# Kernel tuning notes

Measured on AMD Instinct MI355X. Metric: run time of the kernel, lower is better.

Reference implementation:

```python
import jax, jax.numpy as jnp
import numpy as np

N_NODES = 50000
N_GRAPHS = 256

def _gcn_layer(h, src, dst, W, b, n_nodes):
    # GCNConv: linear transform, add self-loops, symmetric deg^-1/2 norm, scatter-add, bias
    h = h @ W  # [N, C_out]
    loop = jnp.arange(n_nodes, dtype=src.dtype)
    src_f = jnp.concatenate([src, loop])
    dst_f = jnp.concatenate([dst, loop])
    ones = jnp.ones_like(dst_f, dtype=h.dtype)
    deg = jax.ops.segment_sum(ones, dst_f, num_segments=n_nodes)  # includes self-loops
    dinv = jnp.where(deg > 0, jax.lax.rsqrt(deg), 0.0)
    norm = dinv[src_f] * dinv[dst_f]  # [E+N]
    msg = h[src_f] * norm[:, None]
    out = jax.ops.segment_sum(msg, dst_f, num_segments=n_nodes)
    return out + b


def setup_inputs() -> dict:
    key = jax.random.key(0)
    ks = jax.random.split(key, 12)
    d_in, d_hid, nhid, nout = 128, 128, 256, 768
    x = jax.random.normal(ks[0], (N_NODES, d_in), dtype=jnp.float32)
    edge_index = jax.random.randint(ks[1], (2, 800000), 0, N_NODES, dtype=jnp.int64)
    batch = jnp.sort(jax.random.randint(ks[2], (N_NODES,), 0, N_GRAPHS, dtype=jnp.int64))
    def lin(k, fan_in, fan_out):
        lim = 1.0 / np.sqrt(fan_in)
        kw, kb = jax.random.split(k)
        W = jax.random.uniform(kw, (fan_in, fan_out), jnp.float32, -lim, lim)
        b = jax.random.uniform(kb, (fan_out,), jnp.float32, -lim, lim)
        return W, b
    W1, b1 = lin(ks[3], d_in, d_hid)
    W2, b2 = lin(ks[4], d_hid, d_hid)
    W3, b3 = lin(ks[5], d_hid, d_hid)
    Wm1, bm1 = lin(ks[6], d_hid, nhid)
    Wm2, bm2 = lin(ks[7], nhid, nout)
    return {"x": x, "edge_index": edge_index, "batch": batch,
            "W1": W1, "b1": b1, "W2": W2, "b2": b2, "W3": W3, "b3": b3,
            "Wm1": Wm1, "bm1": bm1, "Wm2": Wm2, "bm2": bm2}


def reference(x, edge_index, batch, W1, b1, W2, b2, W3, b3, Wm1, bm1, Wm2, bm2):
    src, dst = edge_index[0], edge_index[1]
    n = x.shape[0]
    h = jax.nn.relu(_gcn_layer(x, src, dst, W1, b1, n))
    h = jax.nn.relu(_gcn_layer(h, src, dst, W2, b2, n))
    h = _gcn_layer(h, src, dst, W3, b3, n)  # no relu before pooling (matches source)
    # global mean pool over graphs
    sums = jax.ops.segment_sum(h, batch, num_segments=N_GRAPHS)
    cnts = jax.ops.segment_sum(jnp.ones((n,), h.dtype), batch, num_segments=N_GRAPHS)
    pooled = sums / jnp.clip(cnts, 1.0)[:, None]  # [G, d_hid]
    out = jax.nn.relu(pooled @ Wm1 + bm1)
    out = out @ Wm2 + bm2  # [G, nout]
    return out
```

## Files before the change

kernel.cpp:

```cpp
#include <hip/hip_runtime.h>
#include <hip/hip_bf16.h>

using bf16 = __hip_bfloat16;
typedef __attribute__((ext_vector_type(8))) short bf16x8;
typedef __attribute__((ext_vector_type(4))) float f32x4;

__device__ __forceinline__ float lo2f(unsigned u) { return __uint_as_float(u << 16); }
__device__ __forceinline__ float hi2f(unsigned u) { return __uint_as_float(u & 0xffff0000u); }
__device__ __forceinline__ unsigned pack_bf2(float a, float b) {
    bf16 t0 = __float2bfloat16(a), t1 = __float2bfloat16(b);
    return (unsigned)*(unsigned short*)&t0 | ((unsigned)*(unsigned short*)&t1 << 16);
}

#define CAP 64
#define NPART 8
#define NCHUNK 256

__global__ __launch_bounds__(256)
void fill_pad(const int* __restrict__ ei, int E, int N,
              int* __restrict__ cursor, int* __restrict__ colPad)
{
    int part  = blockIdx.x & (NPART - 1);
    int chunk = blockIdx.x >> 3;
    int lo = (int)(((long long)N * part) >> 3);
    int hi = (int)(((long long)N * (part + 1)) >> 3);
    int csz = (E + NCHUNK - 1) / NCHUNK;
    int beg = chunk * csz;
    int end = min(beg + csz, E);
    const int* __restrict__ dstp = ei + E;
    for (int e = beg + (int)threadIdx.x; e < end; e += 256) {
        int d = __builtin_nontemporal_load(dstp + e);
        if (d >= lo && d < hi) {
            int s = __builtin_nontemporal_load(ei + e);
            int p = atomicAdd(&cursor[d], 1);
            if (p < CAP) colPad[(d << 6) + p] = s;
        }
    }
}

__global__ __launch_bounds__(256)
void dinv_gstart(const int* __restrict__ cursor, int N, float* __restrict__ dinv,
                 const int* __restrict__ batch, int* __restrict__ gstart, int G)
{
    int i = blockIdx.x * 256 + threadIdx.x;
    if (i >= N) return;
    dinv[i] = rsqrtf((float)(cursor[i] + 1));
    int b = batch[i];
    int bp = (i == 0) ? -1 : batch[i - 1];
    for (int q = bp + 1; q <= b; ++q) gstart[q] = i;
    if (i == N - 1)
        for (int q = b + 1; q <= G; ++q) gstart[q] = N;
}

#define LDK 136

__global__ __launch_bounds__(256)
void gemm1_f32(const float* __restrict__ x, const float* __restrict__ W,
               const float* __restrict__ dinv, int N, bf16* __restrict__ g)
{
    __shared__ short Wt[128 * LDK];
    for (int i = threadIdx.x; i < 128 * 128; i += 256) {
        int k = i >> 7, n = i & 127;
        bf16 b = __float2bfloat16(W[i]);
        Wt[n * LDK + k] = *(short*)&b;
    }
    __syncthreads();

    int wave = threadIdx.x >> 6;
    int lane = threadIdx.x & 63;
    int ln   = lane & 15;
    int quad = lane >> 4;
    int m0 = (blockIdx.x * 4 + wave) * 16;
    if (m0 >= N) return;

    int row = m0 + ln;
    if (row >= N) row = N - 1;
    const float* hrow = x + (size_t)row * 128;

    bf16x8 a[4];
#pragma unroll
    for (int kk = 0; kk < 4; ++kk) {
        float4 f0 = *(const float4*)(hrow + kk * 32 + quad * 8);
        float4 f1 = *(const float4*)(hrow + kk * 32 + quad * 8 + 4);
        float fv[8] = {f0.x, f0.y, f0.z, f0.w, f1.x, f1.y, f1.z, f1.w};
#pragma unroll
        for (int j = 0; j < 8; ++j) {
            bf16 tb = __float2bfloat16(fv[j]);
            ((short*)&a[kk])[j] = *(short*)&tb;
        }
    }

    f32x4 c[8];
#pragma unroll
    for (int nt = 0; nt < 8; ++nt) c[nt] = (f32x4){0.f, 0.f, 0.f, 0.f};
#pragma unroll
    for (int kk = 0; kk < 4; ++kk)
#pragma unroll
        for (int nt = 0; nt < 8; ++nt) {
            bf16x8 b = *(const bf16x8*)&Wt[(nt * 16 + ln) * LDK + kk * 32 + quad * 8];
            c[nt] = __builtin_amdgcn_mfma_f32_16x16x32_bf16(a[kk], b, c[nt], 0, 0, 0);
        }
#pragma unroll
    for (int r = 0; r < 4; ++r) {
        int m = m0 + quad * 4 + r;
        if (m < N) {
            float dv = dinv[m];
#pragma unroll
            for (int nt = 0; nt < 8; ++nt) {
                bf16 val = __float2bfloat16(c[nt][r] * dv);
                ((unsigned short*)g)[(size_t)m * 128 + nt * 16 + ln] = *(unsigned short*)&val;
            }
        }
    }
}

__global__ __launch_bounds__(256)
void gemm_mfma(const bf16* __restrict__ hin, const float* __restrict__ W,
               const float* __restrict__ dinv, int N, bf16* __restrict__ g)
{
    __shared__ short Wt[128 * LDK];
    for (int i = threadIdx.x; i < 128 * 128; i += 256) {
        int k = i >> 7, n = i & 127;
        bf16 b = __float2bfloat16(W[i]);
        Wt[n * LDK + k] = *(short*)&b;
    }
    __syncthreads();

    int wave = threadIdx.x >> 6;
    int lane = threadIdx.x & 63;
    int ln   = lane & 15;
    int quad = lane >> 4;
    int m0 = (blockIdx.x * 4 + wave) * 16;
    if (m0 >= N) return;

    int row = m0 + ln;
    if (row >= N) row = N - 1;
    const short* hrow = (const short*)hin + (size_t)row * 128;

    bf16x8 a[4];
#pragma unroll
    for (int kk = 0; kk < 4; ++kk)
        a[kk] = *(const bf16x8*)(hrow + kk * 32 + quad * 8);

    f32x4 c[8];
#pragma unroll
    for (int nt = 0; nt < 8; ++nt) c[nt] = (f32x4){0.f, 0.f, 0.f, 0.f};
#pragma unroll
    for (int kk = 0; kk < 4; ++kk)
#pragma unroll
        for (int nt = 0; nt < 8; ++nt) {
            bf16x8 b = *(const bf16x8*)&Wt[(nt * 16 + ln) * LDK + kk * 32 + quad * 8];
            c[nt] = __builtin_amdgcn_mfma_f32_16x16x32_bf16(a[kk], b, c[nt], 0, 0, 0);
        }
#pragma unroll
    for (int r = 0; r < 4; ++r) {
        int m = m0 + quad * 4 + r;
        if (m < N) {
            float dv = dinv[m];
#pragma unroll
            for (int nt = 0; nt < 8; ++nt) {
                bf16 val = __float2bfloat16(c[nt][r] * dv);
                ((unsigned short*)g)[(size_t)m * 128 + nt * 16 + ln] = *(unsigned short*)&val;
            }
        }
    }
}

__global__ __launch_bounds__(256)
void gather16(const bf16* __restrict__ g, const int* __restrict__ cnt,
              const int* __restrict__ colPad, const float* __restrict__ dinv,
              const float* __restrict__ bias, int N, int do_relu, bf16* __restrict__ hout)
{
    int v = blockIdx.x * 4 + (threadIdx.x >> 6);
    if (v >= N) return;
    int lane = threadIdx.x & 63;
    const unsigned* gp = (const unsigned*)g;

    unsigned su = gp[(size_t)v * 64 + lane];
    float s0 = lo2f(su), s1 = hi2f(su);

    int beg = v << 6;
    int end = beg + min(cnt[v], CAP);
    const int* __restrict__ col = colPad;
    int i = beg;
    for (; i + 8 <= end; i += 8) {
        int cc[8];
#pragma unroll
        for (int j = 0; j < 8; ++j) cc[j] = col[i + j];
        unsigned uu[8];
#pragma unroll
        for (int j = 0; j < 8; ++j) uu[j] = gp[(size_t)cc[j] * 64 + lane];
#pragma unroll
        for (int j = 0; j < 8; ++j) { s0 += lo2f(uu[j]); s1 += hi2f(uu[j]); }
    }
    for (; i + 4 <= end; i += 4) {
        int c0 = col[i], c1 = col[i + 1], c2 = col[i + 2], c3 = col[i + 3];
        unsigned u0 = gp[(size_t)c0 * 64 + lane];
        unsigned u1 = gp[(size_t)c1 * 64 + lane];
        unsigned u2 = gp[(size_t)c2 * 64 + lane];
        unsigned u3 = gp[(size_t)c3 * 64 + lane];
        s0 += lo2f(u0) + lo2f(u1) + lo2f(u2) + lo2f(u3);
        s1 += hi2f(u0) + hi2f(u1) + hi2f(u2) + hi2f(u3);
    }
    for (; i < end; ++i) {
        unsigned u = gp[(size_t)col[i] * 64 + lane];
        s0 += lo2f(u);
        s1 += hi2f(u);
    }
    float dv = dinv[v];
    float2 bb = ((const float2*)bias)[lane];
    float r0 = fmaf(dv, s0, bb.x);
    float r1 = fmaf(dv, s1, bb.y);
    if (do_relu) { r0 = fmaxf(r0, 0.f); r1 = fmaxf(r1, 0.f); }
    ((unsigned*)hout)[(size_t)v * 64 + lane] = pack_bf2(r0, r1);
}

#define PCH 32
__global__ __launch_bounds__(128)
void pool_part(const bf16* __restrict__ h, const int* __restrict__ batch, int N,
               float* __restrict__ pooled)
{
    int c0 = blockIdx.x * PCH;
    if (c0 >= N) return;
    int f = threadIdx.x;
    int end = min(c0 + PCH, N);
    int cur = batch[c0];
    float acc = 0.f;
    for (int v = c0; v < end; ++v) {
        int b = batch[v];
        if (b != cur) {
            atomicAdd(&pooled[cur * 128 + f], acc);
            acc = 0.f;
            cur = b;
        }
        acc += __bfloat162float(h[(size_t)v * 128 + f]);
    }
    atomicAdd(&pooled[cur * 128 + f], acc);
}

__global__ __launch_bounds__(256)
void mlp1g(const float* __restrict__ pooled, const int* __restrict__ gstart,
           const float* __restrict__ Wm1, const float* __restrict__ bm1,
           float* __restrict__ O)
{
    __shared__ float Ps[128];
    int gg = blockIdx.x, j = threadIdx.x;
    if (j < 128) {
        int c = gstart[gg + 1] - gstart[gg];
        Ps[j] = pooled[gg * 128 + j] / (float)(c > 0 ? c : 1);
    }
    __syncthreads();
    float s = 0.f;
#pragma unroll 4
    for (int k = 0; k < 128; ++k) s = fmaf(Ps[k], Wm1[k * 256 + j], s);
    O[(size_t)gg * 256 + j] = fmaxf(s + bm1[j], 0.f);
}

__global__ __launch_bounds__(768)
void mlp2g(const float* __restrict__ O, const float* __restrict__ Wm2,
           const float* __restrict__ bm2, float* __restrict__ out)
{
    __shared__ float Os[256];
    int gg = blockIdx.x, j = threadIdx.x;
    if (j < 256) Os[j] = O[(size_t)gg * 256 + j];
    __syncthreads();
    float s = 0.f;
#pragma unroll 4
    for (int k = 0; k < 256; ++k) s = fmaf(Os[k], Wm2[k * 768 + j], s);
    out[(size_t)gg * 768 + j] = s + bm2[j];
}

extern "C" void kernel_launch(void* const* d_in, const int* in_sizes, int n_in,
                              void* d_out, int out_size, void* d_ws, size_t ws_size,
                              hipStream_t stream)
{
    const float* x     = (const float*)d_in[0];
    const int*   ei    = (const int*)d_in[1];
    const int*   batch = (const int*)d_in[2];
    const float *W1 = (const float*)d_in[3],  *bb1 = (const float*)d_in[4];
    const float *W2 = (const float*)d_in[5],  *bb2 = (const float*)d_in[6];
    const float *W3 = (const float*)d_in[7],  *bb3 = (const float*)d_in[8];
    const float *Wm1 = (const float*)d_in[9],  *bm1 = (const float*)d_in[10];
    const float *Wm2 = (const float*)d_in[11], *bm2 = (const float*)d_in[12];

    const int N = in_sizes[2];
    const int E = in_sizes[1] / 2;
    const int G = out_size / 768;

    char* wp = (char*)d_ws;
    bf16* bufG   = (bf16*)wp;  wp += (size_t)N * 128 * 2;
    bf16* bufH   = (bf16*)wp;  wp += (size_t)N * 128 * 2;
    int*  colPad = (int*)wp;   wp += (size_t)N * CAP * 4;
    int*  cursor = (int*)wp;   wp += (size_t)N * 4;
    float* pooled= (float*)wp; wp += (size_t)G * 128 * 4;
    float* dinv  = (float*)wp; wp += (size_t)N * 4;
    int*  gstart = (int*)wp;   wp += (size_t)(G + 1) * 4;
    float* Obuf  = (float*)wp; wp += (size_t)G * 256 * 4;

    hipMemsetAsync(cursor, 0, (size_t)N * 4 + (size_t)G * 128 * 4, stream);

    const int SB = (N + 255) / 256;
    const int gemm_grid   = (N + 63) / 64;
    const int gather_grid = (N + 3) / 4;

    fill_pad<<<NPART * NCHUNK, 256, 0, stream>>>(ei, E, N, cursor, colPad);
    dinv_gstart<<<SB, 256, 0, stream>>>(cursor, N, dinv, batch, gstart, G);

    gemm1_f32<<<gemm_grid, 256, 0, stream>>>(x, W1, dinv, N, bufG);
    gather16<<<gather_grid, 256, 0, stream>>>(bufG, cursor, colPad, dinv, bb1, N, 1, bufH);
    gemm_mfma<<<gemm_grid, 256, 0, stream>>>(bufH, W2, dinv, N, bufG);
    gather16<<<gather_grid, 256, 0, stream>>>(bufG, cursor, colPad, dinv, bb2, N, 1, bufH);
    gemm_mfma<<<gemm_grid, 256, 0, stream>>>(bufH, W3, dinv, N, bufG);
    gather16<<<gather_grid, 256, 0, stream>>>(bufG, cursor, colPad, dinv, bb3, N, 0, bufH);

    pool_part<<<(N + PCH - 1) / PCH, 128, 0, stream>>>(bufH, batch, N, pooled);
    mlp1g<<<G, 256, 0, stream>>>(pooled, gstart, Wm1, bm1, Obuf);
    mlp2g<<<G, 768, 0, stream>>>(Obuf, Wm2, bm2, (float*)d_out);
}
```

Before: 321.4 us.

## Fuse neighbor aggregation with GEMM by aggregating before the linear transform

Reorders each GCN layer to aggregate dinv-scaled features first and then multiply by W, using A(XW) = (AX)W. This lets the gather and the MFMA GEMM run in one kernel, with each wave aggregating 16 rows into LDS before its matmul. A small scale0 kernel pre-scales x by dinv and casts it to bf16. The aim is to drop three launches and the per-layer bf16 intermediate round trip through global memory. The cost is fewer, longer-running blocks, since each wave gathers 16 nodes serially and the larger LDS use limits occupancy, which may hurt latency hiding for the irregular gathers.

```diff
diff --git a/kernel.cpp b/kernel.cpp
--- a/kernel.cpp
+++ b/kernel.cpp
@@ -52,13 +52,33 @@
         for (int q = b + 1; q <= G; ++q) gstart[q] = N;
 }
 
+__global__ __launch_bounds__(256)
+void scale0(const float* __restrict__ x, const float* __restrict__ dinv,
+            int N, bf16* __restrict__ u)
+{
+    int v = blockIdx.x * 8 + (threadIdx.x >> 5);
+    if (v >= N) return;
+    int l = threadIdx.x & 31;
+    float dv = dinv[v];
+    float4 xx = *(const float4*)(x + (size_t)v * 128 + l * 4);
+    uint2 o;
+    o.x = pack_bf2(xx.x * dv, xx.y * dv);
+    o.y = pack_bf2(xx.z * dv, xx.w * dv);
+    ((uint2*)((unsigned*)u + (size_t)v * 64))[l] = o;
+}
+
 #define LDK 136
-
-__global__ __launch_bounds__(256)
-void gemm1_f32(const float* __restrict__ x, const float* __restrict__ W,
-               const float* __restrict__ dinv, int N, bf16* __restrict__ g)
+#define LDA 68
+
+__global__ __launch_bounds__(256)
+void aggemm(const bf16* __restrict__ uin, const int* __restrict__ cnt,
+            const int* __restrict__ colPad, const float* __restrict__ dinv,
+            const float* __restrict__ W, const float* __restrict__ bias,
+            int N, int do_relu, int out_u, bf16* __restrict__ out)
 {
     __shared__ short Wt[128 * LDK];
+    __shared__ unsigned aggbuf[64 * LDA];
+
     for (int i = threadIdx.x; i < 128 * 128; i += 256) {
         int k = i >> 7, n = i & 127;
         bf16 b = __float2bfloat16(W[i]);
@@ -68,27 +88,56 @@
 
     int wave = threadIdx.x >> 6;
     int lane = threadIdx.x & 63;
+    int m0 = blockIdx.x * 64;
+    const unsigned* up = (const unsigned*)uin;
+
+    for (int i = 0; i < 16; ++i) {
+        int v = m0 + wave * 16 + i;
+        unsigned outw = 0u;
+        if (v < N) {
+            unsigned su = up[(size_t)v * 64 + lane];
+            float s0 = lo2f(su), s1 = hi2f(su);
+            int beg = v << 6;
+            int end = beg + min(cnt[v], CAP);
+            const int* __restrict__ col = colPad;
+            int e = beg;
+            for (; e + 8 <= end; e += 8) {
+                int cc[8];
+#pragma unroll
+                for (int j = 0; j < 8; ++j) cc[j] = col[e + j];
+                unsigned uu[8];
+#pragma unroll
+                for (int j = 0; j < 8; ++j) uu[j] = up[(size_t)cc[j] * 64 + lane];
+#pragma unroll
+                for (int j = 0; j < 8; ++j) { s0 += lo2f(uu[j]); s1 += hi2f(uu[j]); }
+            }
+            for (; e + 4 <= end; e += 4) {
+                int c0 = col[e], c1 = col[e + 1], c2 = col[e + 2], c3 = col[e + 3];
+                unsigned u0 = up[(size_t)c0 * 64 + lane];
+                unsigned u1 = up[(size_t)c1 * 64 + lane];
+                unsigned u2 = up[(size_t)c2 * 64 + lane];
+                unsigned u3 = up[(size_t)c3 * 64 + lane];
+                s0 += lo2f(u0) + lo2f(u1) + lo2f(u2) + lo2f(u3);
+                s1 += hi2f(u0) + hi2f(u1) + hi2f(u2) + hi2f(u3);
+            }
+            for (; e < end; ++e) {
+                unsigned u = up[(size_t)col[e] * 64 + lane];
+                s0 += lo2f(u);
+                s1 += hi2f(u);
+            }
+            outw = pack_bf2(s0, s1);
+        }
+        aggbuf[(wave * 16 + i) * LDA + lane] = outw;
+    }
+
     int ln   = lane & 15;
     int quad = lane >> 4;
-    int m0 = (blockIdx.x * 4 + wave) * 16;
-    if (m0 >= N) return;
-
-    int row = m0 + ln;
-    if (row >= N) row = N - 1;
-    const float* hrow = x + (size_t)row * 128;
 
     bf16x8 a[4];
 #pragma unroll
-    for (int kk = 0; kk < 4; ++kk) {
-        float4 f0 = *(const float4*)(hrow + kk * 32 + quad * 8);
-        float4 f1 = *(const float4*)(hrow + kk * 32 + quad * 8 + 4);
-        float fv[8] = {f0.x, f0.y, f0.z, f0.w, f1.x, f1.y, f1.z, f1.w};
-#pragma unroll
-        for (int j = 0; j < 8; ++j) {
-            bf16 tb = __float2bfloat16(fv[j]);
-            ((short*)&a[kk])[j] = *(short*)&tb;
-        }
-    }
+    for (int kk = 0; kk < 4; ++kk)
+        a[kk] = *(const bf16x8*)((const short*)aggbuf +
+                                 (wave * 16 + ln) * (LDA * 2) + kk * 32 + quad * 8);
 
     f32x4 c[8];
 #pragma unroll
@@ -100,119 +149,22 @@
             bf16x8 b = *(const bf16x8*)&Wt[(nt * 16 + ln) * LDK + kk * 32 + quad * 8];
             c[nt] = __builtin_amdgcn_mfma_f32_16x16x32_bf16(a[kk], b, c[nt], 0, 0, 0);
         }
+
 #pragma unroll
     for (int r = 0; r < 4; ++r) {
-        int m = m0 + quad * 4 + r;
+        int m = m0 + wave * 16 + quad * 4 + r;
         if (m < N) {
             float dv = dinv[m];
 #pragma unroll
             for (int nt = 0; nt < 8; ++nt) {
-                bf16 val = __float2bfloat16(c[nt][r] * dv);
-                ((unsigned short*)g)[(size_t)m * 128 + nt * 16 + ln] = *(unsigned short*)&val;
-            }
-        }
-    }
-}
-
-__global__ __launch_bounds__(256)
-void gemm_mfma(const bf16* __restrict__ hin, const float* __restrict__ W,
-               const float* __restrict__ dinv, int N, bf16* __restrict__ g)
-{
-    __shared__ short Wt[128 * LDK];
-    for (int i = threadIdx.x; i < 128 * 128; i += 256) {
-        int k = i >> 7, n = i & 127;
-        bf16 b = __float2bfloat16(W[i]);
-        Wt[n * LDK + k] = *(short*)&b;
-    }
-    __syncthreads();
-
-    int wave = threadIdx.x >> 6;
-    int lane = threadIdx.x & 63;
-    int ln   = lane & 15;
-    int quad = lane >> 4;
-    int m0 = (blockIdx.x * 4 + wave) * 16;
-    if (m0 >= N) return;
-
-    int row = m0 + ln;
-    if (row >= N) row = N - 1;
-    const short* hrow = (const short*)hin + (size_t)row * 128;
-
-    bf16x8 a[4];
-#pragma unroll
-    for (int kk = 0; kk < 4; ++kk)
-        a[kk] = *(const bf16x8*)(hrow + kk * 32 + quad * 8);
-
-    f32x4 c[8];
-#pragma unroll
-    for (int nt = 0; nt < 8; ++nt) c[nt] = (f32x4){0.f, 0.f, 0.f, 0.f};
-#pragma unroll
-    for (int kk = 0; kk < 4; ++kk)
-#pragma unroll
-        for (int nt = 0; nt < 8; ++nt) {
-            bf16x8 b = *(const bf16x8*)&Wt[(nt * 16 + ln) * LDK + kk * 32 + quad * 8];
-            c[nt] = __builtin_amdgcn_mfma_f32_16x16x32_bf16(a[kk], b, c[nt], 0, 0, 0);
-        }
-#pragma unroll
-    for (int r = 0; r < 4; ++r) {
-        int m = m0 + quad * 4 + r;
-        if (m < N) {
-            float dv = dinv[m];
-#pragma unroll
-            for (int nt = 0; nt < 8; ++nt) {
-                bf16 val = __float2bfloat16(c[nt][r] * dv);
-                ((unsigned short*)g)[(size_t)m * 128 + nt * 16 + ln] = *(unsigned short*)&val;
-            }
-        }
-    }
-}
-
-__global__ __launch_bounds__(256)
-void gather16(const bf16* __restrict__ g, const int* __restrict__ cnt,
-              const int* __restrict__ colPad, const float* __restrict__ dinv,
-              const float* __restrict__ bias, int N, int do_relu, bf16* __restrict__ hout)
-{
-    int v = blockIdx.x * 4 + (threadIdx.x >> 6);
-    if (v >= N) return;
-    int lane = threadIdx.x & 63;
-    const unsigned* gp = (const unsigned*)g;
-
-    unsigned su = gp[(size_t)v * 64 + lane];
-    float s0 = lo2f(su), s1 = hi2f(su);
-
-    int beg = v << 6;
-    int end = beg + min(cnt[v], CAP);
-    const int* __restrict__ col = colPad;
-    int i = beg;
-    for (; i + 8 <= end; i += 8) {
-        int cc[8];
-#pragma unroll
-        for (int j = 0; j < 8; ++j) cc[j] = col[i + j];
-        unsigned uu[8];
-#pragma unroll
-        for (int j = 0; j < 8; ++j) uu[j] = gp[(size_t)cc[j] * 64 + lane];
-#pragma unroll
-        for (int j = 0; j < 8; ++j) { s0 += lo2f(uu[j]); s1 += hi2f(uu[j]); }
-    }
-    for (; i + 4 <= end; i += 4) {
-        int c0 = col[i], c1 = col[i + 1], c2 = col[i + 2], c3 = col[i + 3];
-        unsigned u0 = gp[(size_t)c0 * 64 + lane];
-        unsigned u1 = gp[(size_t)c1 * 64 + lane];
-        unsigned u2 = gp[(size_t)c2 * 64 + lane];
-        unsigned u3 = gp[(size_t)c3 * 64 + lane];
-        s0 += lo2f(u0) + lo2f(u1) + lo2f(u2) + lo2f(u3);
-        s1 += hi2f(u0) + hi2f(u1) + hi2f(u2) + hi2f(u3);
-    }
-    for (; i < end; ++i) {
-        unsigned u = gp[(size_t)col[i] * 64 + lane];
-        s0 += lo2f(u);
-        s1 += hi2f(u);
-    }
-    float dv = dinv[v];
-    float2 bb = ((const float2*)bias)[lane];
-    float r0 = fmaf(dv, s0, bb.x);
-    float r1 = fmaf(dv, s1, bb.y);
-    if (do_relu) { r0 = fmaxf(r0, 0.f); r1 = fmaxf(r1, 0.f); }
-    ((unsigned*)hout)[(size_t)v * 64 + lane] = pack_bf2(r0, r1);
+                float t = fmaf(dv, c[nt][r], bias[nt * 16 + ln]);
+                if (do_relu) t = fmaxf(t, 0.f);
+                if (out_u)   t *= dv;
+                bf16 val = __float2bfloat16(t);
+                ((unsigned short*)out)[(size_t)m * 128 + nt * 16 + ln] = *(unsigned short*)&val;
+            }
+        }
+    }
 }
 
 #define PCH 32
@@ -288,8 +240,8 @@
     const int G = out_size / 768;
 
     char* wp = (char*)d_ws;
-    bf16* bufG   = (bf16*)wp;  wp += (size_t)N * 128 * 2;
-    bf16* bufH   = (bf16*)wp;  wp += (size_t)N * 128 * 2;
+    bf16* bufA   = (bf16*)wp;  wp += (size_t)N * 128 * 2;
+    bf16* bufB   = (bf16*)wp;  wp += (size_t)N * 128 * 2;
     int*  colPad = (int*)wp;   wp += (size_t)N * CAP * 4;
     int*  cursor = (int*)wp;   wp += (size_t)N * 4;
     float* pooled= (float*)wp; wp += (size_t)G * 128 * 4;
@@ -300,20 +252,18 @@
     hipMemsetAsync(cursor, 0, (size_t)N * 4 + (size_t)G * 128 * 4, stream);
 
     const int SB = (N + 255) / 256;
-    const int gemm_grid   = (N + 63) / 64;
-    const int gather_grid = (N + 3) / 4;
+    const int agg_grid = (N + 63) / 64;
 
     fill_pad<<<NPART * NCHUNK, 256, 0, stream>>>(ei, E, N, cursor, colPad);
     dinv_gstart<<<SB, 256, 0, stream>>>(cursor, N, dinv, batch, gstart, G);
 
-    gemm1_f32<<<gemm_grid, 256, 0, stream>>>(x, W1, dinv, N, bufG);
-    gather16<<<gather_grid, 256, 0, stream>>>(bufG, cursor, colPad, dinv, bb1, N, 1, bufH);
-    gemm_mfma<<<gemm_grid, 256, 0, stream>>>(bufH, W2, dinv, N, bufG);
-    gather16<<<gather_grid, 256, 0, stream>>>(bufG, cursor, colPad, dinv, bb2, N, 1, bufH);
-    gemm_mfma<<<gemm_grid, 256, 0, stream>>>(bufH, W3, dinv, N, bufG);
-    gather16<<<gather_grid, 256, 0, stream>>>(bufG, cursor, colPad, dinv, bb3, N, 0, bufH);
-
-    pool_part<<<(N + PCH - 1) / PCH, 128, 0, stream>>>(bufH, batch, N, pooled);
+    scale0<<<(N + 7) / 8, 256, 0, stream>>>(x, dinv, N, bufA);
+
+    aggemm<<<agg_grid, 256, 0, stream>>>(bufA, cursor, colPad, dinv, W1, bb1, N, 1, 1, bufB);
+    aggemm<<<agg_grid, 256, 0, stream>>>(bufB, cursor, colPad, dinv, W2, bb2, N, 1, 1, bufA);
+    aggemm<<<agg_grid, 256, 0, stream>>>(bufA, cursor, colPad, dinv, W3, bb3, N, 0, 0, bufB);
+
+    pool_part<<<(N + PCH - 1) / PCH, 128, 0, stream>>>(bufB, batch, N, pooled);
     mlp1g<<<G, 256, 0, stream>>>(pooled, gstart, Wm1, bm1, Obuf);
     mlp2g<<<G, 768, 0, stream>>>(Obuf, Wm2, bm2, (float*)d_out);
 }
```

Measured after the change: 476.5 us. +48.3%, slower.

## Split neighbor gather into four feature-quarter passes with nontemporal index loads

Applied to the files above, without the earlier changes.

The gather is split into four launches, each covering a 32-feature quarter of every node. In each launch a 16-lane group handles one node, so the gathered working set per pass is 64-byte slices, which may fit better in L2/MALL. Column index loads and output stores are made nontemporal so they do not evict feature data from cache. In exchange, each pass re-reads the whole padded index list, a 64-byte slice under-uses each 128-byte line, and there are three extra launches per layer.

```diff
diff --git a/kernel.cpp b/kernel.cpp
--- a/kernel.cpp
+++ b/kernel.cpp
@@ -167,16 +167,20 @@
 }
 
 __global__ __launch_bounds__(256)
-void gather16(const bf16* __restrict__ g, const int* __restrict__ cnt,
+void gather4q(const bf16* __restrict__ g, const int* __restrict__ cnt,
               const int* __restrict__ colPad, const float* __restrict__ dinv,
-              const float* __restrict__ bias, int N, int do_relu, bf16* __restrict__ hout)
-{
-    int v = blockIdx.x * 4 + (threadIdx.x >> 6);
+              const float* __restrict__ bias, int N, int do_relu, int pass,
+              bf16* __restrict__ hout)
+{
+    int tid = threadIdx.x;
+    int grp = tid >> 4;
+    int l   = tid & 15;
+    int v   = blockIdx.x * 16 + grp;
     if (v >= N) return;
-    int lane = threadIdx.x & 63;
     const unsigned* gp = (const unsigned*)g;
-
-    unsigned su = gp[(size_t)v * 64 + lane];
+    int qoff = pass * 16 + l;
+
+    unsigned su = gp[(size_t)v * 64 + qoff];
     float s0 = lo2f(su), s1 = hi2f(su);
 
     int beg = v << 6;
@@ -186,33 +190,37 @@
     for (; i + 8 <= end; i += 8) {
         int cc[8];
 #pragma unroll
-        for (int j = 0; j < 8; ++j) cc[j] = col[i + j];
+        for (int j = 0; j < 8; ++j) cc[j] = __builtin_nontemporal_load(col + i + j);
         unsigned uu[8];
 #pragma unroll
-        for (int j = 0; j < 8; ++j) uu[j] = gp[(size_t)cc[j] * 64 + lane];
+        for (int j = 0; j < 8; ++j) uu[j] = gp[(size_t)cc[j] * 64 + qoff];
 #pragma unroll
         for (int j = 0; j < 8; ++j) { s0 += lo2f(uu[j]); s1 += hi2f(uu[j]); }
     }
     for (; i + 4 <= end; i += 4) {
-        int c0 = col[i], c1 = col[i + 1], c2 = col[i + 2], c3 = col[i + 3];
-        unsigned u0 = gp[(size_t)c0 * 64 + lane];
-        unsigned u1 = gp[(size_t)c1 * 64 + lane];
-        unsigned u2 = gp[(size_t)c2 * 64 + lane];
-        unsigned u3 = gp[(size_t)c3 * 64 + lane];
+        int c0 = __builtin_nontemporal_load(col + i);
+        int c1 = __builtin_nontemporal_load(col + i + 1);
+        int c2 = __builtin_nontemporal_load(col + i + 2);
+        int c3 = __builtin_nontemporal_load(col + i + 3);
+        unsigned u0 = gp[(size_t)c0 * 64 + qoff];
+        unsigned u1 = gp[(size_t)c1 * 64 + qoff];
+        unsigned u2 = gp[(size_t)c2 * 64 + qoff];
+        unsigned u3 = gp[(size_t)c3 * 64 + qoff];
         s0 += lo2f(u0) + lo2f(u1) + lo2f(u2) + lo2f(u3);
         s1 += hi2f(u0) + hi2f(u1) + hi2f(u2) + hi2f(u3);
     }
     for (; i < end; ++i) {
-        unsigned u = gp[(size_t)col[i] * 64 + lane];
+        unsigned u = gp[(size_t)__builtin_nontemporal_load(col + i) * 64 + qoff];
         s0 += lo2f(u);
         s1 += hi2f(u);
     }
     float dv = dinv[v];
-    float2 bb = ((const float2*)bias)[lane];
+    float2 bb = ((const float2*)bias)[qoff];
     float r0 = fmaf(dv, s0, bb.x);
     float r1 = fmaf(dv, s1, bb.y);
     if (do_relu) { r0 = fmaxf(r0, 0.f); r1 = fmaxf(r1, 0.f); }
-    ((unsigned*)hout)[(size_t)v * 64 + lane] = pack_bf2(r0, r1);
+    __builtin_nontemporal_store(pack_bf2(r0, r1),
+                                (unsigned*)hout + (size_t)v * 64 + qoff);
 }
 
 #define PCH 32
@@ -300,18 +308,21 @@
     hipMemsetAsync(cursor, 0, (size_t)N * 4 + (size_t)G * 128 * 4, stream);
 
     const int SB = (N + 255) / 256;
-    const int gemm_grid   = (N + 63) / 64;
-    const int gather_grid = (N + 3) / 4;
+    const int gemm_grid = (N + 63) / 64;
+    const int g4_grid   = (N + 15) / 16;
 
     fill_pad<<<NPART * NCHUNK, 256, 0, stream>>>(ei, E, N, cursor, colPad);
     dinv_gstart<<<SB, 256, 0, stream>>>(cursor, N, dinv, batch, gstart, G);
 
     gemm1_f32<<<gemm_grid, 256, 0, stream>>>(x, W1, dinv, N, bufG);
-    gather16<<<gather_grid, 256, 0, stream>>>(bufG, cursor, colPad, dinv, bb1, N, 1, bufH);
+    for (int p = 0; p < 4; ++p)
+        gather4q<<<g4_grid, 256, 0, stream>>>(bufG, cursor, colPad, dinv, bb1, N, 1, p, bufH);
     gemm_mfma<<<gemm_grid, 256, 0, stream>>>(bufH, W2, dinv, N, bufG);
-    gather16<<<gather_grid, 256, 0, stream>>>(bufG, cursor, colPad, dinv, bb2, N, 1, bufH);
+    for (int p = 0; p < 4; ++p)
+        gather4q<<<g4_grid, 256, 0, stream>>>(bufG, cursor, colPad, dinv, bb2, N, 1, p, bufH);
     gemm_mfma<<<gemm_grid, 256, 0, stream>>>(bufH, W3, dinv, N, bufG);
-    gather16<<<gather_grid, 256, 0, stream>>>(bufG, cursor, colPad, dinv, bb3, N, 0, bufH);
+    for (int p = 0; p < 4; ++p)
+        gather4q<<<g4_grid, 256, 0, stream>>>(bufG, cursor, colPad, dinv, bb3, N, 0, p, bufH);
 
     pool_part<<<(N + PCH - 1) / PCH, 128, 0, stream>>>(bufH, batch, N, pooled);
     mlp1g<<<G, 256, 0, stream>>>(pooled, gstart, Wm1, bm1, Obuf);
```

Measured after the change: 449.0 us. 39.7% more time.
